# Performance work log

Measured on AMD Instinct MI355X. Metric: run time of the kernel, lower is better.

The kernel has to match this reference:

```python
import jax, jax.numpy as jnp
import numpy as np

B, M, D = 256, 256, 16
H1, H2 = 64, 64
HN = H1 // 2  # split_half keeps first half as next-layer state


def setup_inputs() -> dict:
    key = jax.random.key(0)
    ks = jax.random.split(key, 8)
    x = jax.random.normal(ks[0], (B, M), dtype=jnp.float32)
    emb = 0.02 * jax.random.normal(ks[1], (M, D), dtype=jnp.float32)  # field_embedding
    # Conv1d(kernel=1) weights squeezed to [out_ch, in_ch]
    def xavier(k, o, i):
        lim = np.sqrt(6.0 / (o + i)).astype(np.float32)
        return jax.random.uniform(k, (o, i), dtype=jnp.float32, minval=-lim, maxval=lim)
    W0 = xavier(ks[2], H1, M * M)      # layer 0: in_ch = m*m
    b0 = jnp.zeros((H1,), dtype=jnp.float32)
    W1 = xavier(ks[3], H2, HN * M)     # layer 1: in_ch = (H1//2)*m
    b1 = jnp.zeros((H2,), dtype=jnp.float32)
    out_width = (H1 - HN) + H2         # 32 + 64 = 96
    fcW = xavier(ks[4], 2, out_width)
    fcb = jnp.zeros((2,), dtype=jnp.float32)
    return {"x": x, "emb": emb, "W0": W0, "b0": b0, "W1": W1, "b1": b1, "fcW": fcW, "fcb": fcb}


def _cin_layer(Xk_prev, X0, W, b):
    # outer product over fields, flattened: Z [B, prev_H*m, d]
    Bd = X0.shape[0]
    Z = jnp.einsum('bhd,bmd->bhmd', Xk_prev, X0).reshape(Bd, -1, X0.shape[-1])
    # kernel-1 Conv1d == channel-mixing matmul per d slice, + bias, + relu
    return jax.nn.relu(jnp.einsum('bcd,oc->bod', Z, W) + b[None, :, None])


def reference(x, emb, W0, b0, W1, b1, fcW, fcb):
    X0 = jnp.einsum('bi,ij->bij', x, emb)          # [B, m, d]
    X1 = _cin_layer(X0, X0, W0, b0)                # [B, H1, d]
    out1 = X1[:, HN:, :]                            # direct output half
    Xp = X1[:, :HN, :]                              # hidden half feeds next layer
    X2 = _cin_layer(Xp, X0, W1, b1)                # [B, H2, d] (last layer: full output)
    cin_out = jnp.concatenate([out1.sum(axis=2), X2.sum(axis=2)], axis=1)  # [B, 96]
    return cin_out @ fcW.T + fcb
```

## Files before the change

kernel.cpp:

```cpp
#include <hip/hip_runtime.h>

typedef unsigned short u16;
typedef short bf16x8 __attribute__((ext_vector_type(8)));
typedef float f32x4 __attribute__((ext_vector_type(4)));

#define AS1 __attribute__((address_space(1)))
#define AS3 __attribute__((address_space(3)))

__device__ __forceinline__ u16 f2bf(float f) {
    unsigned u = __float_as_uint(f);
    u += 0x7fffu + ((u >> 16) & 1u);
    return (u16)(u >> 16);
}
__device__ __forceinline__ float bf2f(u16 h) {
    return __uint_as_float(((unsigned)h) << 16);
}

__device__ __forceinline__ void gload_lds16(const void* g, void* l) {
    __builtin_amdgcn_global_load_lds((AS1 unsigned int*)(g),
                                     (AS3 unsigned int*)(l), 16, 0, 0);
}

__global__ void prep_kernel(const float* __restrict__ W0, const float* __restrict__ W1,
                            const float* __restrict__ x, const float* __restrict__ emb,
                            u16* __restrict__ W0b, u16* __restrict__ W1b,
                            u16* __restrict__ Qt, u16* __restrict__ E1) {
    int gid = blockIdx.x;
    if (gid < 4608) {
        int i = gid * 256 + threadIdx.x;
        const float* src; u16* dst; int j;
        if (i < 1048576) { src = W0; dst = W0b; j = i; }
        else             { src = W1; dst = W1b; j = i - 1048576; }
        float4 v = reinterpret_cast<const float4*>(src)[j];
        ushort4 o;
        o.x = f2bf(v.x); o.y = f2bf(v.y); o.z = f2bf(v.z); o.w = f2bf(v.w);
        reinterpret_cast<ushort4*>(dst)[j] = o;
    } else {
        int n = (gid - 4608) * 4 + (threadIdx.x >> 6);
        int lane = threadIdx.x & 63;
        int b = n >> 4, d = n & 15;
        int m0 = lane * 4;
        float4 xv = *reinterpret_cast<const float4*>(x + b * 256 + m0);
        ushort4 q;
        q.x = f2bf(xv.x * emb[(m0 + 0) * 16 + d]);
        q.y = f2bf(xv.y * emb[(m0 + 1) * 16 + d]);
        q.z = f2bf(xv.z * emb[(m0 + 2) * 16 + d]);
        q.w = f2bf(xv.w * emb[(m0 + 3) * 16 + d]);
        *reinterpret_cast<ushort4*>(Qt + n * 256 + m0) = q;
        int e1 = (n >> 7) * 32768 + (m0 >> 6) * 8192 + ((n >> 6) & 1) * 4096
               + ((m0 >> 4) & 3) * 1024 + ((n >> 4) & 3) * 256
               + (((m0 >> 2) & 3) * 16 + (n & 15)) * 4;
        *reinterpret_cast<ushort4*>(E1 + e1) = q;
    }
}

__global__ __launch_bounds__(512, 4) void cin1_kernel(
    const u16* __restrict__ W0b, const u16* __restrict__ Qt, const u16* __restrict__ E1,
    const float* __restrict__ b0, u16* __restrict__ E2, float* __restrict__ S1)
{
    __shared__ __attribute__((aligned(16))) u16 As[3][8192];
    __shared__ __attribute__((aligned(16))) u16 Bs[3][4096];
    __shared__ float part[4][128];

    const int tid = threadIdx.x, lane = tid & 63, w = tid >> 6;
    const int wh = w >> 1, wn = w & 1;
    const int bid = blockIdx.x;
    const int g8 = bid & 7, rest = bid >> 3;
    const int o = g8 * 8 + (rest & 7);
    const int ntile = rest >> 3;

    const int rl = lane >> 2;
    const int sw = ((lane & 3) ^ ((rl + (rl >> 2)) & 3)) << 3;
    const u16* aS0 = W0b + (o * 256 + (w * 2 + 0) * 16 + rl) * 256 + sw;
    const u16* aS1 = W0b + (o * 256 + (w * 2 + 1) * 16 + rl) * 256 + sw;
    const u16* bS0 = Qt + (ntile * 128 + w * 16 + rl) * 256 + sw;
    const int ldsA0 = (w * 2 + 0) * 512, ldsA1 = (w * 2 + 1) * 512;
    const int ldsB0 = w * 512;

    const int rbA = wh * 64 + (lane & 15);
    const int rbB = wn * 64 + (lane & 15);
    const int sl = lane >> 4;
    const int aOff = rbA * 32 + ((sl ^ ((rbA + (rbA >> 2)) & 3)) << 3);
    const int bOff = rbB * 32 + ((sl ^ ((rbB + (rbB >> 2)) & 3)) << 3);

    f32x4 zero = {0.f, 0.f, 0.f, 0.f};
    f32x4 acc[4][4];
#pragma unroll
    for (int f = 0; f < 4; ++f)
#pragma unroll
        for (int gg = 0; gg < 4; ++gg) acc[f][gg] = zero;

    auto stage = [&](int kc, int bb) {
        int ko = kc * 32;
        gload_lds16(aS0 + ko, &As[bb][ldsA0]);
        gload_lds16(aS1 + ko, &As[bb][ldsA1]);
        gload_lds16(bS0 + ko, &Bs[bb][ldsB0]);
    };

    stage(0, 0); stage(1, 1);
#pragma unroll
    for (int kc = 0; kc < 8; ++kc) {
        if (kc < 7) asm volatile("s_waitcnt vmcnt(3)" ::: "memory");
        else        asm volatile("s_waitcnt vmcnt(0)" ::: "memory");
        __builtin_amdgcn_s_barrier();
        asm volatile("" ::: "memory");
        if (kc < 6) stage(kc + 2, (kc + 2) % 3);
        const u16* Ab = &As[kc % 3][0];
        const u16* Bb = &Bs[kc % 3][0];
        bf16x8 a[4], b[4];
#pragma unroll
        for (int f = 0; f < 4; ++f)
            a[f] = *reinterpret_cast<const bf16x8*>(Ab + aOff + f * 512);
#pragma unroll
        for (int gg = 0; gg < 4; ++gg)
            b[gg] = *reinterpret_cast<const bf16x8*>(Bb + bOff + gg * 512);
        __builtin_amdgcn_s_setprio(1);
#pragma unroll
        for (int f = 0; f < 4; ++f)
#pragma unroll
            for (int gg = 0; gg < 4; ++gg)
                acc[f][gg] = __builtin_amdgcn_mfma_f32_16x16x32_bf16(a[f], b[gg], acc[f][gg], 0, 0, 0);
        __builtin_amdgcn_s_setprio(0);
    }

    float psum[4] = {0.f, 0.f, 0.f, 0.f};
    const u16* eb = E1 + ntile * 32768 + wh * 8192 + wn * 4096 + lane * 4;
#pragma unroll
    for (int f = 0; f < 4; ++f)
#pragma unroll
        for (int gg = 0; gg < 4; ++gg) {
            ushort4 wv = *reinterpret_cast<const ushort4*>(eb + f * 1024 + gg * 256);
            psum[gg] += bf2f(wv.x) * acc[f][gg][0] + bf2f(wv.y) * acc[f][gg][1]
                      + bf2f(wv.z) * acc[f][gg][2] + bf2f(wv.w) * acc[f][gg][3];
        }
#pragma unroll
    for (int gg = 0; gg < 4; ++gg) {
        float p = psum[gg];
        p += __shfl_xor(p, 16);
        p += __shfl_xor(p, 32);
        if (lane < 16) part[wh][wn * 64 + gg * 16 + lane] = p;
    }
    __syncthreads();
    if (tid < 128) {
        const int nl = tid;
        float v = part[0][nl] + part[1][nl] + part[2][nl] + part[3][nl] + b0[o];
        float r = fmaxf(v, 0.0f);
        const int n = ntile * 128 + nl;
        if (o < 32) {
            E2[((ntile * 2 + (nl >> 6)) * 4 + ((nl >> 4) & 3)) * 512 + (nl & 15) * 32 + o] = f2bf(r);
        } else {
            float s = r;
            s += __shfl_xor(s, 1); s += __shfl_xor(s, 2);
            s += __shfl_xor(s, 4); s += __shfl_xor(s, 8);
            if ((nl & 15) == 0) S1[(n >> 4) * 32 + (o - 32)] = s;
        }
    }
}

__global__ __launch_bounds__(256, 4) void cin2_kernel(
    const u16* __restrict__ W1b, const u16* __restrict__ Qt, const u16* __restrict__ E2,
    const float* __restrict__ b1, float* __restrict__ S2)
{
    __shared__ __attribute__((aligned(16))) u16 As[3][4096];
    __shared__ __attribute__((aligned(16))) u16 Bs[3][4096];
    __shared__ float part[2][2][128];

    const int tid = threadIdx.x, lane = tid & 63, w = tid >> 6;
    const int wh = w >> 1, wn = w & 1;
    const int bid = blockIdx.x;
    const int g8 = bid & 7, rest = bid >> 3;
    const int og = g8 * 2 + (rest & 1);
    const int ntile = rest >> 1;

    const int rl = lane >> 2;
    const int sw = ((lane & 3) ^ ((rl + (rl >> 2)) & 3)) << 3;
    const u16* aS0 = W1b + (og * 128 + (w * 2 + 0) * 16 + rl) * 256 + sw;
    const u16* aS1 = W1b + (og * 128 + (w * 2 + 1) * 16 + rl) * 256 + sw;
    const u16* bS0 = Qt + (ntile * 128 + (w * 2 + 0) * 16 + rl) * 256 + sw;
    const u16* bS1 = Qt + (ntile * 128 + (w * 2 + 1) * 16 + rl) * 256 + sw;
    const int ldsI0 = (w * 2 + 0) * 512, ldsI1 = (w * 2 + 1) * 512;

    const int rbA = wh * 64 + (lane & 15);
    const int rbB = wn * 64 + (lane & 15);
    const int sl = lane >> 4;
    const int aOff = rbA * 32 + ((sl ^ ((rbA + (rbA >> 2)) & 3)) << 3);
    const int bOff = rbB * 32 + ((sl ^ ((rbB + (rbB >> 2)) & 3)) << 3);

    f32x4 zero = {0.f, 0.f, 0.f, 0.f};
    f32x4 acc[4][4];
#pragma unroll
    for (int f = 0; f < 4; ++f)
#pragma unroll
        for (int gg = 0; gg < 4; ++gg) acc[f][gg] = zero;

    auto stage = [&](int kc, int bb) {
        int ko = kc * 32;
        gload_lds16(aS0 + ko, &As[bb][ldsI0]);
        gload_lds16(aS1 + ko, &As[bb][ldsI1]);
        gload_lds16(bS0 + ko, &Bs[bb][ldsI0]);
        gload_lds16(bS1 + ko, &Bs[bb][ldsI1]);
    };

    stage(0, 0); stage(1, 1);
#pragma unroll
    for (int kc = 0; kc < 8; ++kc) {
        if (kc < 7) asm volatile("s_waitcnt vmcnt(4)" ::: "memory");
        else        asm volatile("s_waitcnt vmcnt(0)" ::: "memory");
        __builtin_amdgcn_s_barrier();
        asm volatile("" ::: "memory");
        if (kc < 6) stage(kc + 2, (kc + 2) % 3);
        const u16* Ab = &As[kc % 3][0];
        const u16* Bb = &Bs[kc % 3][0];
        bf16x8 a[4], b[4];
#pragma unroll
        for (int f = 0; f < 4; ++f)
            a[f] = *reinterpret_cast<const bf16x8*>(Ab + aOff + f * 512);
#pragma unroll
        for (int gg = 0; gg < 4; ++gg)
            b[gg] = *reinterpret_cast<const bf16x8*>(Bb + bOff + gg * 512);
        __builtin_amdgcn_s_setprio(1);
#pragma unroll
        for (int f = 0; f < 4; ++f)
#pragma unroll
            for (int gg = 0; gg < 4; ++gg)
                acc[f][gg] = __builtin_amdgcn_mfma_f32_16x16x32_bf16(a[f], b[gg], acc[f][gg], 0, 0, 0);
        __builtin_amdgcn_s_setprio(0);
    }

    float psum[2][4] = {{0.f,0.f,0.f,0.f},{0.f,0.f,0.f,0.f}};
    const u16* eb = E2 + (ntile * 2 + wn) * 2048 + (lane & 15) * 32 + (lane >> 4) * 4;
#pragma unroll
    for (int f = 0; f < 4; ++f)
#pragma unroll
        for (int gg = 0; gg < 4; ++gg) {
            ushort4 wv = *reinterpret_cast<const ushort4*>(eb + gg * 512 + (f & 1) * 16);
            psum[f >> 1][gg] += bf2f(wv.x) * acc[f][gg][0] + bf2f(wv.y) * acc[f][gg][1]
                              + bf2f(wv.z) * acc[f][gg][2] + bf2f(wv.w) * acc[f][gg][3];
        }
#pragma unroll
    for (int ol = 0; ol < 2; ++ol)
#pragma unroll
        for (int gg = 0; gg < 4; ++gg) {
            float p = psum[ol][gg];
            p += __shfl_xor(p, 16);
            p += __shfl_xor(p, 32);
            if (lane < 16) part[wh][ol][wn * 64 + gg * 16 + lane] = p;
        }
    __syncthreads();
    if (tid < 128) {
        const int nl = tid;
        const int n = ntile * 128 + nl;
#pragma unroll
        for (int o4 = 0; o4 < 4; ++o4) {
            const int oo = og * 4 + o4;
            float v = part[o4 >> 1][o4 & 1][nl] + b1[oo];
            float r = fmaxf(v, 0.0f);
            float s = r;
            s += __shfl_xor(s, 1); s += __shfl_xor(s, 2);
            s += __shfl_xor(s, 4); s += __shfl_xor(s, 8);
            if ((nl & 15) == 0) S2[(n >> 4) * 64 + oo] = s;
        }
    }
}

__global__ void final_fc_kernel(const float* __restrict__ S1, const float* __restrict__ S2,
                                const float* __restrict__ fcW, const float* __restrict__ fcb,
                                float* __restrict__ out) {
    int b = threadIdx.x;
    float a0 = fcb[0], a1 = fcb[1];
#pragma unroll 8
    for (int c = 0; c < 32; ++c) {
        float v = S1[b * 32 + c];
        a0 += v * fcW[c]; a1 += v * fcW[96 + c];
    }
#pragma unroll 8
    for (int c = 0; c < 64; ++c) {
        float v = S2[b * 64 + c];
        a0 += v * fcW[32 + c]; a1 += v * fcW[96 + 32 + c];
    }
    out[b * 2 + 0] = a0;
    out[b * 2 + 1] = a1;
}

extern "C" void kernel_launch(void* const* d_in, const int* in_sizes, int n_in,
                              void* d_out, int out_size, void* d_ws, size_t ws_size,
                              hipStream_t stream) {
    const float* x   = (const float*)d_in[0];
    const float* emb = (const float*)d_in[1];
    const float* W0  = (const float*)d_in[2];
    const float* b0  = (const float*)d_in[3];
    const float* W1  = (const float*)d_in[4];
    const float* b1  = (const float*)d_in[5];
    const float* fcW = (const float*)d_in[6];
    const float* fcb = (const float*)d_in[7];
    float* out = (float*)d_out;

    char* ws = (char*)d_ws;
    u16*   W0b = (u16*)(ws);
    u16*   W1b = (u16*)(ws + 8388608);
    u16*   Qt  = (u16*)(ws + 9437184);
    u16*   E1  = (u16*)(ws + 11534336);
    u16*   E2  = (u16*)(ws + 13631488);
    float* S1  = (float*)(ws + 13893632);
    float* S2  = (float*)(ws + 13926400);

    prep_kernel<<<5632, 256, 0, stream>>>(W0, W1, x, emb, W0b, W1b, Qt, E1);
    cin1_kernel<<<2048, 512, 0, stream>>>(W0b, Qt, E1, b0, E2, S1);
    cin2_kernel<<<512, 256, 0, stream>>>(W1b, Qt, E2, b1, S2);
    final_fc_kernel<<<1, 256, 0, stream>>>(S1, S2, fcW, fcb, out);
}
```

Measured before the change: 71.64 us.

## Enlarge cin1 tile to 256x256 with 8-phase ping-pong MFMA schedule

```diff
diff --git a/kernel.cpp b/kernel.cpp
--- a/kernel.cpp
+++ b/kernel.cpp
@@ -47,112 +47,143 @@
         q.z = f2bf(xv.z * emb[(m0 + 2) * 16 + d]);
         q.w = f2bf(xv.w * emb[(m0 + 3) * 16 + d]);
         *reinterpret_cast<ushort4*>(Qt + n * 256 + m0) = q;
-        int e1 = (n >> 7) * 32768 + (m0 >> 6) * 8192 + ((n >> 6) & 1) * 4096
-               + ((m0 >> 4) & 3) * 1024 + ((n >> 4) & 3) * 256
+        int e1 = (n >> 8) * 65536 + (m0 >> 7) * 32768 + ((n >> 6) & 3) * 8192
+               + ((m0 >> 4) & 7) * 1024 + ((n >> 4) & 3) * 256
                + (((m0 >> 2) & 3) * 16 + (n & 15)) * 4;
         *reinterpret_cast<ushort4*>(E1 + e1) = q;
     }
 }
 
-__global__ __launch_bounds__(512, 4) void cin1_kernel(
+__global__ __launch_bounds__(512, 2) void cin1_kernel(
     const u16* __restrict__ W0b, const u16* __restrict__ Qt, const u16* __restrict__ E1,
     const float* __restrict__ b0, u16* __restrict__ E2, float* __restrict__ S1)
 {
-    __shared__ __attribute__((aligned(16))) u16 As[3][8192];
-    __shared__ __attribute__((aligned(16))) u16 Bs[3][4096];
-    __shared__ float part[4][128];
+    __shared__ __attribute__((aligned(16))) u16 lds[2][2][2][8192];
+    __shared__ float part[2][256];
 
     const int tid = threadIdx.x, lane = tid & 63, w = tid >> 6;
-    const int wh = w >> 1, wn = w & 1;
+    const int wm = w >> 2, wn = w & 3;
     const int bid = blockIdx.x;
-    const int g8 = bid & 7, rest = bid >> 3;
-    const int o = g8 * 8 + (rest & 7);
-    const int ntile = rest >> 3;
-
-    const int rl = lane >> 2;
-    const int sw = ((lane & 3) ^ ((rl + (rl >> 2)) & 3)) << 3;
-    const u16* aS0 = W0b + (o * 256 + (w * 2 + 0) * 16 + rl) * 256 + sw;
-    const u16* aS1 = W0b + (o * 256 + (w * 2 + 1) * 16 + rl) * 256 + sw;
-    const u16* bS0 = Qt + (ntile * 128 + w * 16 + rl) * 256 + sw;
-    const int ldsA0 = (w * 2 + 0) * 512, ldsA1 = (w * 2 + 1) * 512;
-    const int ldsB0 = w * 512;
-
-    const int rbA = wh * 64 + (lane & 15);
-    const int rbB = wn * 64 + (lane & 15);
-    const int sl = lane >> 4;
-    const int aOff = rbA * 32 + ((sl ^ ((rbA + (rbA >> 2)) & 3)) << 3);
-    const int bOff = rbB * 32 + ((sl ^ ((rbB + (rbB >> 2)) & 3)) << 3);
+    const int o = (bid & 7) * 8 + ((bid >> 3) & 7);
+    const int ntile = bid >> 6;
+
+    const int srl = lane >> 3;
+    const int ssw = ((lane & 7) ^ srl) * 8;
+    const u16* aG = W0b + (o * 256 + w * 16 + srl) * 256 + ssw;
+    const u16* bG = Qt + (ntile * 256 + w * 16 + srl) * 256 + ssw;
+    const int ldsW = w * 1024;
+
+    const int c15 = lane & 15;
+    const int ph0s = (((lane >> 4) + 0) ^ (lane & 7)) * 8;
+    const int ph1s = (((lane >> 4) + 4) ^ (lane & 7)) * 8;
+    const u16* aB = &lds[0][0][wm][0] + c15 * 64;
+    const u16* bB = &lds[0][1][wn >> 1][0] + (wn & 1) * 4096 + c15 * 64;
 
     f32x4 zero = {0.f, 0.f, 0.f, 0.f};
-    f32x4 acc[4][4];
-#pragma unroll
-    for (int f = 0; f < 4; ++f)
-#pragma unroll
-        for (int gg = 0; gg < 4; ++gg) acc[f][gg] = zero;
-
-    auto stage = [&](int kc, int bb) {
-        int ko = kc * 32;
-        gload_lds16(aS0 + ko, &As[bb][ldsA0]);
-        gload_lds16(aS1 + ko, &As[bb][ldsA1]);
-        gload_lds16(bS0 + ko, &Bs[bb][ldsB0]);
-    };
-
-    stage(0, 0); stage(1, 1);
-#pragma unroll
-    for (int kc = 0; kc < 8; ++kc) {
-        if (kc < 7) asm volatile("s_waitcnt vmcnt(3)" ::: "memory");
-        else        asm volatile("s_waitcnt vmcnt(0)" ::: "memory");
-        __builtin_amdgcn_s_barrier();
-        asm volatile("" ::: "memory");
-        if (kc < 6) stage(kc + 2, (kc + 2) % 3);
-        const u16* Ab = &As[kc % 3][0];
-        const u16* Bb = &Bs[kc % 3][0];
-        bf16x8 a[4], b[4];
-#pragma unroll
-        for (int f = 0; f < 4; ++f)
-            a[f] = *reinterpret_cast<const bf16x8*>(Ab + aOff + f * 512);
-#pragma unroll
-        for (int gg = 0; gg < 4; ++gg)
-            b[gg] = *reinterpret_cast<const bf16x8*>(Bb + bOff + gg * 512);
-        __builtin_amdgcn_s_setprio(1);
-#pragma unroll
-        for (int f = 0; f < 4; ++f)
-#pragma unroll
-            for (int gg = 0; gg < 4; ++gg)
-                acc[f][gg] = __builtin_amdgcn_mfma_f32_16x16x32_bf16(a[f], b[gg], acc[f][gg], 0, 0, 0);
-        __builtin_amdgcn_s_setprio(0);
-    }
+    f32x4 acc[8][4];
+#pragma unroll
+    for (int f = 0; f < 8; ++f)
+#pragma unroll
+        for (int g = 0; g < 4; ++g) acc[f][g] = zero;
+
+    bf16x8 aR[4][2], bR[4][2];
+
+#define STAGE(op, half, kt, buf)                                                          \
+    {                                                                                     \
+        const u16* s_ = (op) ? bG : aG;                                                   \
+        gload_lds16(s_ + (half) * 32768 + (kt) * 64, &lds[buf][op][half][ldsW]);          \
+        gload_lds16(s_ + (half) * 32768 + 2048 + (kt) * 64, &lds[buf][op][half][ldsW + 512]); \
+    }
+#define READ_A(buf, mh)                                                                   \
+    _Pragma("unroll") for (int j_ = 0; j_ < 4; ++j_) {                                    \
+        aR[j_][0] = *reinterpret_cast<const bf16x8*>(aB + (buf) * 32768 + ((mh) * 4 + j_) * 1024 + ph0s); \
+        aR[j_][1] = *reinterpret_cast<const bf16x8*>(aB + (buf) * 32768 + ((mh) * 4 + j_) * 1024 + ph1s); \
+    }
+#define READ_B01(buf)                                                                     \
+    _Pragma("unroll") for (int j_ = 0; j_ < 2; ++j_) {                                    \
+        bR[j_][0] = *reinterpret_cast<const bf16x8*>(bB + (buf) * 32768 + j_ * 1024 + ph0s); \
+        bR[j_][1] = *reinterpret_cast<const bf16x8*>(bB + (buf) * 32768 + j_ * 1024 + ph1s); \
+    }
+#define READ_B23(buf)                                                                     \
+    _Pragma("unroll") for (int j_ = 0; j_ < 2; ++j_) {                                    \
+        bR[2 + j_][0] = *reinterpret_cast<const bf16x8*>(bB + (buf) * 32768 + (2 + j_) * 1024 + ph0s); \
+        bR[2 + j_][1] = *reinterpret_cast<const bf16x8*>(bB + (buf) * 32768 + (2 + j_) * 1024 + ph1s); \
+    }
+#define BARF() { __builtin_amdgcn_s_barrier(); asm volatile("" ::: "memory"); }
+#define MFMA_Q(mh, nh)                                                                    \
+    __builtin_amdgcn_sched_barrier(0);                                                    \
+    __builtin_amdgcn_s_setprio(1);                                                        \
+    _Pragma("unroll") for (int j_ = 0; j_ < 4; ++j_)                                      \
+    _Pragma("unroll") for (int k_ = 0; k_ < 2; ++k_)                                      \
+    _Pragma("unroll") for (int ks_ = 0; ks_ < 2; ++ks_)                                   \
+        acc[(mh) * 4 + j_][(nh) * 2 + k_] = __builtin_amdgcn_mfma_f32_16x16x32_bf16(      \
+            aR[j_][ks_], bR[(nh) * 2 + k_][ks_], acc[(mh) * 4 + j_][(nh) * 2 + k_], 0, 0, 0); \
+    __builtin_amdgcn_s_setprio(0);                                                        \
+    __builtin_amdgcn_sched_barrier(0);
+
+    STAGE(0, 0, 0, 0) STAGE(0, 1, 0, 0) STAGE(1, 0, 0, 0) STAGE(1, 1, 0, 0)
+    STAGE(0, 0, 1, 1) STAGE(0, 1, 1, 1) STAGE(1, 0, 1, 1) STAGE(1, 1, 1, 1)
+    asm volatile("s_waitcnt vmcnt(8)" ::: "memory");
+    BARF();
+
+    READ_A(0, 0) READ_B01(0)                         BARF(); MFMA_Q(0, 0) BARF();
+    READ_B23(0)                                      BARF(); MFMA_Q(0, 1) BARF();
+    READ_A(0, 1) STAGE(1, 0, 2, 0)                   BARF(); MFMA_Q(1, 1) BARF();
+    STAGE(1, 1, 2, 0) STAGE(0, 0, 2, 0)
+    asm volatile("s_waitcnt vmcnt(6)" ::: "memory");
+    BARF(); MFMA_Q(1, 0) BARF();
+    READ_A(1, 0) READ_B01(1) STAGE(0, 1, 2, 0)       BARF(); MFMA_Q(0, 0) BARF();
+    READ_B23(1)                                      BARF(); MFMA_Q(0, 1) BARF();
+    READ_A(1, 1)                                     BARF(); MFMA_Q(1, 1) BARF();
+    asm volatile("s_waitcnt vmcnt(0)" ::: "memory");
+    BARF(); MFMA_Q(1, 0) BARF();
+
+    READ_A(0, 0) READ_B01(0) STAGE(0, 0, 3, 1) STAGE(0, 1, 3, 1) BARF(); MFMA_Q(0, 0) BARF();
+    READ_B23(0) STAGE(1, 0, 3, 1) STAGE(1, 1, 3, 1)              BARF(); MFMA_Q(0, 1) BARF();
+    READ_A(0, 1)                                                 BARF(); MFMA_Q(1, 1) BARF();
+    asm volatile("s_waitcnt vmcnt(0)" ::: "memory");
+    BARF(); MFMA_Q(1, 0) BARF();
+    READ_A(1, 0) READ_B01(1)                                     BARF(); MFMA_Q(0, 0) BARF();
+    READ_B23(1)                                                  BARF(); MFMA_Q(0, 1) BARF();
+    READ_A(1, 1)                                                 BARF(); MFMA_Q(1, 1) BARF();
+    BARF(); MFMA_Q(1, 0)
+
+#undef STAGE
+#undef READ_A
+#undef READ_B01
+#undef READ_B23
+#undef MFMA_Q
 
     float psum[4] = {0.f, 0.f, 0.f, 0.f};
-    const u16* eb = E1 + ntile * 32768 + wh * 8192 + wn * 4096 + lane * 4;
-#pragma unroll
-    for (int f = 0; f < 4; ++f)
-#pragma unroll
-        for (int gg = 0; gg < 4; ++gg) {
-            ushort4 wv = *reinterpret_cast<const ushort4*>(eb + f * 1024 + gg * 256);
-            psum[gg] += bf2f(wv.x) * acc[f][gg][0] + bf2f(wv.y) * acc[f][gg][1]
-                      + bf2f(wv.z) * acc[f][gg][2] + bf2f(wv.w) * acc[f][gg][3];
-        }
-#pragma unroll
-    for (int gg = 0; gg < 4; ++gg) {
-        float p = psum[gg];
+    const u16* eb = E1 + ntile * 65536 + wm * 32768 + wn * 8192 + lane * 4;
+#pragma unroll
+    for (int f = 0; f < 8; ++f)
+#pragma unroll
+        for (int g = 0; g < 4; ++g) {
+            ushort4 wv = *reinterpret_cast<const ushort4*>(eb + f * 1024 + g * 256);
+            psum[g] += bf2f(wv.x) * acc[f][g][0] + bf2f(wv.y) * acc[f][g][1]
+                     + bf2f(wv.z) * acc[f][g][2] + bf2f(wv.w) * acc[f][g][3];
+        }
+#pragma unroll
+    for (int g = 0; g < 4; ++g) {
+        float p = psum[g];
         p += __shfl_xor(p, 16);
         p += __shfl_xor(p, 32);
-        if (lane < 16) part[wh][wn * 64 + gg * 16 + lane] = p;
+        if (lane < 16) part[wm][wn * 64 + g * 16 + lane] = p;
     }
     __syncthreads();
-    if (tid < 128) {
+    if (tid < 256) {
         const int nl = tid;
-        float v = part[0][nl] + part[1][nl] + part[2][nl] + part[3][nl] + b0[o];
+        float v = part[0][nl] + part[1][nl] + b0[o];
         float r = fmaxf(v, 0.0f);
-        const int n = ntile * 128 + nl;
+        const int n = ntile * 256 + nl;
         if (o < 32) {
-            E2[((ntile * 2 + (nl >> 6)) * 4 + ((nl >> 4) & 3)) * 512 + (nl & 15) * 32 + o] = f2bf(r);
+            E2[(n >> 4) * 512 + (n & 15) * 32 + o] = f2bf(r);
         } else {
             float s = r;
             s += __shfl_xor(s, 1); s += __shfl_xor(s, 2);
             s += __shfl_xor(s, 4); s += __shfl_xor(s, 8);
-            if ((nl & 15) == 0) S1[(n >> 4) * 32 + (o - 32)] = s;
+            if ((n & 15) == 0) S1[(n >> 4) * 32 + (o - 32)] = s;
         }
     }
 }
@@ -305,7 +336,7 @@
     float* S2  = (float*)(ws + 13926400);
 
     prep_kernel<<<5632, 256, 0, stream>>>(W0, W1, x, emb, W0b, W1b, Qt, E1);
-    cin1_kernel<<<2048, 512, 0, stream>>>(W0b, Qt, E1, b0, E2, S1);
+    cin1_kernel<<<1024, 512, 0, stream>>>(W0b, Qt, E1, b0, E2, S1);
     cin2_kernel<<<512, 256, 0, stream>>>(W1b, Qt, E2, b1, S2);
     final_fc_kernel<<<1, 256, 0, stream>>>(S1, S2, fcW, fcb, out);
 }
```

Result: slower. 73.75 us (+2.9%).
